# Kernel tuning notes

Hardware: AMD Instinct MI355X
Metric: run time of the kernel (lower is better)

The kernel has to match this reference:

```python
import jax, jax.numpy as jnp
import numpy as np

N = 100000          # nodes
E = 3_200_000       # edges (avg degree 32)
F_IN = 1433
H1, C1 = 8, 8       # conv1: 8 heads x 8 channels -> 64 concat
H2, C2 = 1, 7       # conv2: 1 head x 7 classes
NEG_SLOPE = 0.2


def setup_inputs() -> dict:
    key = jax.random.key(0)
    ks = jax.random.split(key, 10)
    x = jax.random.normal(ks[0], (N, F_IN), dtype=jnp.float32)
    edge_index = jax.random.randint(ks[1], (2, E), 0, N, dtype=jnp.int64)
    s1 = 1.0 / np.sqrt(F_IN)
    s2 = 1.0 / np.sqrt(H1 * C1)
    return {
        "x": x,
        "edge_index": edge_index,
        "W1": jax.random.normal(ks[2], (F_IN, H1 * C1), dtype=jnp.float32) * s1,
        "att_src1": jax.random.normal(ks[3], (H1, C1), dtype=jnp.float32) * s2,
        "att_dst1": jax.random.normal(ks[4], (H1, C1), dtype=jnp.float32) * s2,
        "b1": jnp.zeros((H1 * C1,), dtype=jnp.float32),
        "W2": jax.random.normal(ks[5], (H1 * C1, H2 * C2), dtype=jnp.float32) * s2,
        "att_src2": jax.random.normal(ks[6], (H2, C2), dtype=jnp.float32),
        "att_dst2": jax.random.normal(ks[7], (H2, C2), dtype=jnp.float32),
        "b2": jnp.zeros((H2 * C2,), dtype=jnp.float32),
    }


def gat_conv(x, src, dst, W, att_src, att_dst, b, heads, ch):
    # x: [N, F_in]; src/dst: [E'] (self-loops already appended)
    h = (x @ W).reshape(N, heads, ch)                     # [N, H, C]
    a_src = jnp.einsum('nhc,hc->nh', h, att_src)          # [N, H]
    a_dst = jnp.einsum('nhc,hc->nh', h, att_dst)
    e = a_src[src] + a_dst[dst]                           # [E', H]
    e = jax.nn.leaky_relu(e, NEG_SLOPE)
    # segment softmax over incoming edges of each dst node
    m = jax.ops.segment_max(e, dst, num_segments=N)       # [N, H]
    w = jnp.exp(e - m[dst])
    denom = jax.ops.segment_sum(w, dst, num_segments=N)   # [N, H]
    alpha = w / denom[dst]                                # [E', H]
    msg = alpha[:, :, None] * h[src]                      # [E', H, C]
    out = jax.ops.segment_sum(msg, dst, num_segments=N)   # [N, H, C]
    return out.reshape(N, heads * ch) + b


def reference(x, edge_index, W1, att_src1, att_dst1, b1, W2, att_src2, att_dst2, b2):
    loops = jnp.arange(N, dtype=edge_index.dtype)
    src = jnp.concatenate([edge_index[0], loops])
    dst = jnp.concatenate([edge_index[1], loops])
    # eval mode: all dropout layers are identity
    h = gat_conv(x, src, dst, W1, att_src1, att_dst1, b1, H1, C1)   # [N, 64]
    h = jax.nn.elu(h)
    h = gat_conv(h, src, dst, W2, att_src2, att_dst2, b2, H2, C2)   # [N, 7]
    return jax.nn.log_softmax(h, axis=1)
```

## Files before the change

### kernel.cpp

```cpp
#include <hip/hip_runtime.h>
#include <hip/hip_bf16.h>
#include <math.h>

#define NN 100000
#define EE 3200000
#define ET (EE + NN)
#define FIN 1433
#define KPAD 1440
#define NT 45
#define F1 64
#define F2 7
#define NB 391
#define G1B 782
#define SB 1024
#define CAP 128

typedef __attribute__((ext_vector_type(8))) short short8;
typedef __attribute__((ext_vector_type(4))) float f32x4;
typedef __attribute__((address_space(3))) unsigned int u32_lds;
typedef __attribute__((address_space(1))) const unsigned int u32_glb;

static __device__ __forceinline__ unsigned short f2bf(float f) {
  __hip_bfloat16 h = __float2bfloat16(f);
  return *reinterpret_cast<unsigned short*>(&h);
}
static __device__ __forceinline__ float bf2f(unsigned short u) {
  return __uint_as_float((unsigned int)u << 16);
}

__global__ __launch_bounds__(256) void k_prep(const float* __restrict__ W1,
                                              int* __restrict__ cnt,
                                              unsigned short* __restrict__ WT) {
  int i = blockIdx.x * 256 + threadIdx.x;
  if (i < NN) cnt[i] = 0;
  if (i < F1 * KPAD) {
    int c = i / KPAD, k = i - c * KPAD;
    WT[i] = f2bf((k < FIN) ? W1[k * F1 + c] : 0.f);
  }
}

#define BM 128
#define TILEA 16384
#define TILEB 4096
#define BUFB (TILEA + TILEB)

__global__ __launch_bounds__(256) void k_fuse1(const float* __restrict__ X,
                                               const unsigned short* __restrict__ WT,
                                               unsigned short* __restrict__ Hb,
                                               const int* __restrict__ ei,
                                               int* __restrict__ cnt,
                                               int* __restrict__ csr) {
  if (blockIdx.x >= G1B) {
    const int stride = SB * 256;
    for (int e = (blockIdx.x - G1B) * 256 + threadIdx.x; e < ET; e += stride) {
      int src, dst;
      if (e < EE) { src = ei[e]; dst = ei[EE + e]; }
      else        { src = e - EE; dst = src; }
      int pos = atomicAdd(&cnt[dst], 1);
      csr[(dst << 7) + pos] = src;
    }
    return;
  }
  __shared__ __align__(16) char smem[2 * BUFB];
  const int tid = threadIdx.x;
  const int lane = tid & 63;
  const int wid = tid >> 6;
  const int row0 = blockIdx.x * BM;
  const int wr = (wid >> 1) * 64;
  const int wc = (wid & 1) * 32;
  const int l15 = lane & 15, l4 = lane >> 4;

  const int lrq = tid >> 3;
  const int mq = tid & 7;
  const char* Xb = (const char*)X;
  size_t aoff[4];
#pragma unroll
  for (int q = 0; q < 4; ++q) {
    int lr = q * 32 + lrq;
    int gr = row0 + lr; if (gr >= NN) gr = NN - 1;
    int c = mq ^ (lr & 7);
    aoff[q] = (size_t)gr * (FIN * 4) + (size_t)c * 16;
  }
  const unsigned short* bsrc =
      WT + (tid >> 2) * KPAD + (((tid & 3) ^ ((tid >> 3) & 3)) << 3);

  f32x4 acc[4][2];
#pragma unroll
  for (int a = 0; a < 4; ++a)
#pragma unroll
    for (int b = 0; b < 2; ++b) acc[a][b] = 0.f;

  auto gstage = [&](int k0, char* buf) {
#pragma unroll
    for (int q = 0; q < 4; ++q) {
      __builtin_amdgcn_global_load_lds(
          (u32_glb*)(Xb + aoff[q] + (size_t)k0 * 4),
          (u32_lds*)(buf + q * 4096 + wid * 1024), 16, 0, 0);
    }
  };

  gstage(0, smem);
  {
    short8 b0 = *(const short8*)(bsrc + 0);
    *(short8*)(smem + TILEA + tid * 16) = b0;
  }
  __syncthreads();

  int cur = 0;
  for (int t = 0; t < NT; ++t) {
    char* buf = smem + cur * BUFB;
    char* nbuf = smem + (cur ^ 1) * BUFB;
    const bool have_next = (t + 1 < NT);
    const bool tail = (t + 1 == NT - 1);
    short8 bnext;
    f32x4 atail[4];
    if (have_next) {
      if (!tail) {
        gstage((t + 1) * 32, nbuf);
      } else {
#pragma unroll
        for (int q = 0; q < 4; ++q) {
          int lr = q * 32 + lrq;
          int gr = row0 + lr; if (gr >= NN) gr = NN - 1;
          int c = mq ^ (lr & 7);
          int kb = (NT - 1) * 32 + c * 4;
          const float* xp = X + (size_t)gr * FIN + kb;
#pragma unroll
          for (int j = 0; j < 4; ++j)
            atail[q][j] = (kb + j < FIN) ? xp[j] : 0.f;
        }
      }
      bnext = *(const short8*)(bsrc + (t + 1) * 32);
    }

    short8 af[4], bf[2];
    const int sz = l15 & 7;
#pragma unroll
    for (int fr = 0; fr < 4; ++fr) {
      int r = wr + fr * 16 + l15;
      f32x4 a0 = *(const f32x4*)(buf + r * 128 + ((2 * l4) ^ sz) * 16);
      f32x4 a1 = *(const f32x4*)(buf + r * 128 + ((2 * l4 + 1) ^ sz) * 16);
      short8 v;
#pragma unroll
      for (int j = 0; j < 4; ++j) {
        v[j] = (short)f2bf(a0[j]);
        v[4 + j] = (short)f2bf(a1[j]);
      }
      af[fr] = v;
    }
#pragma unroll
    for (int fc = 0; fc < 2; ++fc) {
      int c = wc + fc * 16 + l15;
      int jp = l4 ^ ((c >> 1) & 3);
      bf[fc] = *(const short8*)(buf + TILEA + c * 64 + jp * 16);
    }
#pragma unroll
    for (int fr = 0; fr < 4; ++fr)
#pragma unroll
      for (int fc = 0; fc < 2; ++fc)
        acc[fr][fc] = __builtin_amdgcn_mfma_f32_16x16x32_bf16(
            af[fr], bf[fc], acc[fr][fc], 0, 0, 0);

    if (have_next) {
      if (tail) {
#pragma unroll
        for (int q = 0; q < 4; ++q)
          *(f32x4*)(nbuf + (q * 32 + lrq) * 128 + mq * 16) = atail[q];
      }
      *(short8*)(nbuf + TILEA + tid * 16) = bnext;
    }
    __syncthreads();
    cur ^= 1;
  }

#pragma unroll
  for (int fr = 0; fr < 4; ++fr) {
    int rbase = row0 + wr + fr * 16 + l4 * 4;
#pragma unroll
    for (int q = 0; q < 4; ++q) {
      int r = rbase + q;
      if (r < NN) {
#pragma unroll
        for (int fc = 0; fc < 2; ++fc)
          Hb[(size_t)r * F1 + wc + fc * 16 + l15] = f2bf(acc[fr][fc][q]);
      }
    }
  }
}

__global__ __launch_bounds__(256) void k_att1(const unsigned short* __restrict__ Hb,
                                              const float* __restrict__ attS,
                                              const float* __restrict__ attD,
                                              float* __restrict__ aS,
                                              float* __restrict__ aD) {
  __shared__ float s_s[64], s_d[64];
  if (threadIdx.x < 64) { s_s[threadIdx.x] = attS[threadIdx.x]; s_d[threadIdx.x] = attD[threadIdx.x]; }
  __syncthreads();
  int idx = blockIdx.x * 256 + threadIdx.x;
  int n = idx >> 3, h = idx & 7;
  if (n >= NN) return;
  short8 v8 = *(const short8*)(Hb + (size_t)n * 64 + h * 8);
  float ss = 0.f, dd = 0.f;
#pragma unroll
  for (int c = 0; c < 8; ++c) {
    float v = bf2f((unsigned short)v8[c]);
    ss = fmaf(v, s_s[h * 8 + c], ss);
    dd = fmaf(v, s_d[h * 8 + c], dd);
  }
  aS[n * 8 + h] = ss;
  aD[n * 8 + h] = dd;
}

__global__ __launch_bounds__(256) void k_agg1(const unsigned short* __restrict__ Hb,
                                              const float* __restrict__ aS,
                                              const float* __restrict__ aD,
                                              const int* __restrict__ cnt,
                                              const int* __restrict__ csr,
                                              const float* __restrict__ b1,
                                              const float* __restrict__ W2,
                                              const float* __restrict__ s2,
                                              const float* __restrict__ d2,
                                              unsigned short* __restrict__ H2b,
                                              float* __restrict__ aD2) {
  __shared__ float s_w2[448];
  __shared__ float s_ss[7], s_dd[7];
  __shared__ float s_b1[64];
  for (int i = threadIdx.x; i < 448; i += 256) s_w2[i] = W2[i];
  if (threadIdx.x < 7) { s_ss[threadIdx.x] = s2[threadIdx.x]; s_dd[threadIdx.x] = d2[threadIdx.x]; }
  if (threadIdx.x < 64) s_b1[threadIdx.x] = b1[threadIdx.x];
  __syncthreads();

  const int wv = threadIdx.x >> 6, lane = threadIdx.x & 63;
  const int n = blockIdx.x * 4 + wv;
  if (n >= NN) return;
  const int eg = lane >> 3, q = lane & 7;
  const float adv = aD[n * 8 + q];
  const int beg = n << 7;
  const int deg = cnt[n];
  float acc[8] = {};
  float den = 0.f;
#pragma unroll 2
  for (int i = eg; i < deg; i += 8) {
    int s = csr[beg + i];
    float e = aS[s * 8 + q] + adv;
    e = (e > 0.f) ? e : 0.2f * e;
    float w = __expf(e);
    den += w;
    short8 hv = *(const short8*)(Hb + (size_t)s * 64 + q * 8);
#pragma unroll
    for (int c = 0; c < 8; ++c)
      acc[c] = fmaf(w, bf2f((unsigned short)hv[c]), acc[c]);
  }
#pragma unroll
  for (int off = 8; off < 64; off <<= 1) {
    den += __shfl_xor(den, off, 64);
#pragma unroll
    for (int c = 0; c < 8; ++c) acc[c] += __shfl_xor(acc[c], off, 64);
  }
  if (eg == 0) {
    float inv = 1.f / den;
    float v[8];
#pragma unroll
    for (int c = 0; c < 8; ++c) {
      float t = acc[c] * inv + s_b1[q * 8 + c];
      v[c] = (t > 0.f) ? t : (__expf(t) - 1.f);
    }
    float p[7] = {};
#pragma unroll
    for (int c = 0; c < 8; ++c) {
      const float* wr = &s_w2[(q * 8 + c) * 7];
#pragma unroll
      for (int j = 0; j < 7; ++j) p[j] = fmaf(v[c], wr[j], p[j]);
    }
#pragma unroll
    for (int off = 1; off < 8; off <<= 1) {
#pragma unroll
      for (int j = 0; j < 7; ++j) p[j] += __shfl_xor(p[j], off, 64);
    }
    if (q == 0) {
      float s = 0.f, d = 0.f;
      short8 row;
#pragma unroll
      for (int j = 0; j < 7; ++j) {
        row[j] = (short)f2bf(p[j]);
        s = fmaf(p[j], s_ss[j], s);
        d = fmaf(p[j], s_dd[j], d);
      }
      row[7] = (short)f2bf(s);
      *(short8*)(H2b + (size_t)n * 8) = row;
      aD2[n] = d;
    }
  }
}

__global__ __launch_bounds__(256) void k_agg2(const unsigned short* __restrict__ H2b,
                                              const float* __restrict__ aD2,
                                              const int* __restrict__ cnt,
                                              const int* __restrict__ csr,
                                              const float* __restrict__ b2,
                                              float* __restrict__ out) {
  const int wv = threadIdx.x >> 6, lane = threadIdx.x & 63;
  const int n = blockIdx.x * 4 + wv;
  if (n >= NN) return;
  const float adv = aD2[n];
  const int beg = n << 7;
  const int deg = cnt[n];
  float acc[7] = {};
  float den = 0.f;
  for (int j = lane; j < deg; j += 64) {
    int s = csr[beg + j];
    short8 hv = *(const short8*)(H2b + (size_t)s * 8);
    float e = bf2f((unsigned short)hv[7]) + adv;
    e = (e > 0.f) ? e : 0.2f * e;
    float wgt = __expf(e);
    den += wgt;
#pragma unroll
    for (int c = 0; c < 7; ++c)
      acc[c] = fmaf(wgt, bf2f((unsigned short)hv[c]), acc[c]);
  }
#pragma unroll
  for (int off = 32; off > 0; off >>= 1) {
    den += __shfl_xor(den, off, 64);
#pragma unroll
    for (int c = 0; c < 7; ++c) acc[c] += __shfl_xor(acc[c], off, 64);
  }
  if (lane == 0) {
    float inv = 1.f / den;
    float v[7];
    float m = -1e30f;
#pragma unroll
    for (int c = 0; c < 7; ++c) { v[c] = acc[c] * inv + b2[c]; m = fmaxf(m, v[c]); }
    float se = 0.f;
#pragma unroll
    for (int c = 0; c < 7; ++c) se += __expf(v[c] - m);
    float lse = m + __logf(se);
#pragma unroll
    for (int c = 0; c < 7; ++c) out[n * 7 + c] = v[c] - lse;
  }
}

extern "C" void kernel_launch(void* const* d_in, const int* in_sizes, int n_in,
                              void* d_out, int out_size, void* d_ws, size_t ws_size,
                              hipStream_t stream) {
  const float* x   = (const float*)d_in[0];
  const int*   ei  = (const int*)d_in[1];
  const float* W1  = (const float*)d_in[2];
  const float* as1 = (const float*)d_in[3];
  const float* ad1 = (const float*)d_in[4];
  const float* b1  = (const float*)d_in[5];
  const float* W2  = (const float*)d_in[6];
  const float* as2 = (const float*)d_in[7];
  const float* ad2 = (const float*)d_in[8];
  const float* b2  = (const float*)d_in[9];
  float* out = (float*)d_out;

  char* ws = (char*)d_ws;
  size_t off = 0;
  auto alloc = [&](size_t bytes) {
    void* p = ws + off;
    off += (bytes + 255) & ~(size_t)255;
    return p;
  };
  unsigned short* h1b = (unsigned short*)alloc((size_t)NN * 64 * 2);
  float* sc1    = (float*)alloc((size_t)NN * 8 * 4);
  float* dc1    = (float*)alloc((size_t)NN * 8 * 4);
  unsigned short* h2b = (unsigned short*)alloc((size_t)NN * 8 * 2);
  float* dc2    = (float*)alloc((size_t)NN * 4);
  int*   cnt    = (int*)alloc((size_t)NN * 4);
  int*   csr    = (int*)alloc((size_t)NN * CAP * 4);
  unsigned short* w1t = (unsigned short*)alloc((size_t)F1 * KPAD * 2);

  k_prep<<<NB, 256, 0, stream>>>(W1, cnt, w1t);

  k_fuse1<<<G1B + SB, 256, 0, stream>>>(x, w1t, h1b, ei, cnt, csr);

  k_att1<<<(NN * 8 + 255) / 256, 256, 0, stream>>>(h1b, as1, ad1, sc1, dc1);

  k_agg1<<<(NN + 3) / 4, 256, 0, stream>>>(h1b, sc1, dc1, cnt, csr, b1,
                                           W2, as2, ad2, h2b, dc2);

  k_agg2<<<(NN + 3) / 4, 256, 0, stream>>>(h2b, dc2, cnt, csr, b2, out);
}
```

Measured before the change: 438.6 us.

## Partition CSR build per XCD with workgroup-scope atomics, merge in fused att kernel

The edge-bucketing phase now reads the XCC id from a hardware register and writes into one of eight per-XCD count/CSR arrays. It uses workgroup-scope atomics on the assumption that each partition is only touched by blocks on one XCD, which keeps the atomics in the local L2 instead of device-coherent memory. A new merge phase, fused into the attention-score kernel as extra blocks, concatenates the eight partitions into the original CSR layout. The risks are the extra merge pass and memory, a per-partition cap of 24 that could overflow for high-degree nodes, and relying on workgroup-scope atomics being coherent across CUs within an XCD.

```diff
diff --git a/kernel.cpp b/kernel.cpp
--- a/kernel.cpp
+++ b/kernel.cpp
@@ -14,6 +14,10 @@
 #define G1B 782
 #define SB 1024
 #define CAP 128
+#define NXCD 8
+#define CAPX 24
+#define A1B 3125
+#define CPB 25000
 
 typedef __attribute__((ext_vector_type(8))) short short8;
 typedef __attribute__((ext_vector_type(4))) float f32x4;
@@ -29,10 +33,10 @@
 }
 
 __global__ __launch_bounds__(256) void k_prep(const float* __restrict__ W1,
-                                              int* __restrict__ cnt,
+                                              int* __restrict__ cnt2,
                                               unsigned short* __restrict__ WT) {
   int i = blockIdx.x * 256 + threadIdx.x;
-  if (i < NN) cnt[i] = 0;
+  if (i < NXCD * NN) cnt2[i] = 0;
   if (i < F1 * KPAD) {
     int c = i / KPAD, k = i - c * KPAD;
     WT[i] = f2bf((k < FIN) ? W1[k * F1 + c] : 0.f);
@@ -48,16 +52,22 @@
                                                const unsigned short* __restrict__ WT,
                                                unsigned short* __restrict__ Hb,
                                                const int* __restrict__ ei,
-                                               int* __restrict__ cnt,
-                                               int* __restrict__ csr) {
+                                               int* __restrict__ cnt2,
+                                               int* __restrict__ csr2) {
   if (blockIdx.x >= G1B) {
+    int xcc;
+    asm volatile("s_getreg_b32 %0, hwreg(20, 0, 32)" : "=s"(xcc));
+    xcc &= 7;
+    int* mycnt = cnt2 + xcc * NN;
+    int* mycsr = csr2 + (size_t)xcc * NN * CAPX;
     const int stride = SB * 256;
     for (int e = (blockIdx.x - G1B) * 256 + threadIdx.x; e < ET; e += stride) {
       int src, dst;
       if (e < EE) { src = ei[e]; dst = ei[EE + e]; }
       else        { src = e - EE; dst = src; }
-      int pos = atomicAdd(&cnt[dst], 1);
-      csr[(dst << 7) + pos] = src;
+      int pos = __hip_atomic_fetch_add(&mycnt[dst], 1, __ATOMIC_RELAXED,
+                                       __HIP_MEMORY_SCOPE_WORKGROUP);
+      mycsr[dst * CAPX + pos] = src;
     }
     return;
   }
@@ -188,11 +198,31 @@
   }
 }
 
-__global__ __launch_bounds__(256) void k_att1(const unsigned short* __restrict__ Hb,
-                                              const float* __restrict__ attS,
-                                              const float* __restrict__ attD,
-                                              float* __restrict__ aS,
-                                              float* __restrict__ aD) {
+__global__ __launch_bounds__(256) void k_fuse2(const unsigned short* __restrict__ Hb,
+                                               const float* __restrict__ attS,
+                                               const float* __restrict__ attD,
+                                               float* __restrict__ aS,
+                                               float* __restrict__ aD,
+                                               const int* __restrict__ cnt2,
+                                               const int* __restrict__ csr2,
+                                               int* __restrict__ cnt,
+                                               int* __restrict__ csr) {
+  if (blockIdx.x >= A1B) {
+    const int wv = threadIdx.x >> 6, lane = threadIdx.x & 63;
+    const int n = (blockIdx.x - A1B) * 4 + wv;
+    if (n >= NN) return;
+    int c[NXCD];
+    int deg = 0;
+#pragma unroll
+    for (int x = 0; x < NXCD; ++x) { c[x] = cnt2[x * NN + n]; deg += c[x]; }
+    for (int i = lane; i < deg; i += 64) {
+      int x = 0, off = i;
+      while (off >= c[x]) { off -= c[x]; ++x; }
+      csr[(n << 7) + i] = csr2[((size_t)x * NN + n) * CAPX + off];
+    }
+    if (lane == 0) cnt[n] = deg;
+    return;
+  }
   __shared__ float s_s[64], s_d[64];
   if (threadIdx.x < 64) { s_s[threadIdx.x] = attS[threadIdx.x]; s_d[threadIdx.x] = attD[threadIdx.x]; }
   __syncthreads();
@@ -368,13 +398,16 @@
   float* dc2    = (float*)alloc((size_t)NN * 4);
   int*   cnt    = (int*)alloc((size_t)NN * 4);
   int*   csr    = (int*)alloc((size_t)NN * CAP * 4);
+  int*   cnt2   = (int*)alloc((size_t)NXCD * NN * 4);
+  int*   csr2   = (int*)alloc((size_t)NXCD * NN * CAPX * 4);
   unsigned short* w1t = (unsigned short*)alloc((size_t)F1 * KPAD * 2);
 
-  k_prep<<<NB, 256, 0, stream>>>(W1, cnt, w1t);
-
-  k_fuse1<<<G1B + SB, 256, 0, stream>>>(x, w1t, h1b, ei, cnt, csr);
-
-  k_att1<<<(NN * 8 + 255) / 256, 256, 0, stream>>>(h1b, as1, ad1, sc1, dc1);
+  k_prep<<<(NXCD * NN + 255) / 256, 256, 0, stream>>>(W1, cnt2, w1t);
+
+  k_fuse1<<<G1B + SB, 256, 0, stream>>>(x, w1t, h1b, ei, cnt2, csr2);
+
+  k_fuse2<<<A1B + CPB, 256, 0, stream>>>(h1b, as1, ad1, sc1, dc1,
+                                         cnt2, csr2, cnt, csr);
 
   k_agg1<<<(NN + 3) / 4, 256, 0, stream>>>(h1b, sc1, dc1, cnt, csr, b1,
                                            W2, as2, ad2, h2b, dc2);
```

Result: slower. 482.7 us (+10.0%).

## Build CSR via two-level binning instead of global atomics scatter

Applied to the files above, without the earlier changes.

Replaces the global-atomic CSR build (one atomicAdd per edge on a per-node counter, with scattered writes) with a two-pass bucketed sort. Each block first builds a shared-memory histogram of 512-node bins, then a single-block scan turns these into offsets. A binning kernel writes packed (local dst, src) words into contiguous bin regions, and per-bin blocks build the CSR rows using LDS atomics, fused with the attention-score kernel. The aim is to remove global atomic contention and random writes, at the cost of extra launches, a serial scan kernel and an extra pass over the edges.

```diff
diff --git a/kernel.cpp b/kernel.cpp
--- a/kernel.cpp
+++ b/kernel.cpp
@@ -10,10 +10,13 @@
 #define NT 45
 #define F1 64
 #define F2 7
-#define NB 391
 #define G1B 782
-#define SB 1024
 #define CAP 128
+#define BINS 200
+#define SB1 256
+#define CH_E 12891
+#define NB4 196
+#define A1B 3125
 
 typedef __attribute__((ext_vector_type(8))) short short8;
 typedef __attribute__((ext_vector_type(4))) float f32x4;
@@ -29,10 +32,8 @@
 }
 
 __global__ __launch_bounds__(256) void k_prep(const float* __restrict__ W1,
-                                              int* __restrict__ cnt,
                                               unsigned short* __restrict__ WT) {
   int i = blockIdx.x * 256 + threadIdx.x;
-  if (i < NN) cnt[i] = 0;
   if (i < F1 * KPAD) {
     int c = i / KPAD, k = i - c * KPAD;
     WT[i] = f2bf((k < FIN) ? W1[k * F1 + c] : 0.f);
@@ -48,17 +49,19 @@
                                                const unsigned short* __restrict__ WT,
                                                unsigned short* __restrict__ Hb,
                                                const int* __restrict__ ei,
-                                               int* __restrict__ cnt,
-                                               int* __restrict__ csr) {
+                                               int* __restrict__ histM) {
   if (blockIdx.x >= G1B) {
-    const int stride = SB * 256;
-    for (int e = (blockIdx.x - G1B) * 256 + threadIdx.x; e < ET; e += stride) {
-      int src, dst;
-      if (e < EE) { src = ei[e]; dst = ei[EE + e]; }
-      else        { src = e - EE; dst = src; }
-      int pos = atomicAdd(&cnt[dst], 1);
-      csr[(dst << 7) + pos] = src;
-    }
+    __shared__ int hist[BINS];
+    const int b = blockIdx.x - G1B;
+    for (int i = threadIdx.x; i < BINS; i += 256) hist[i] = 0;
+    __syncthreads();
+    const int e0 = b * CH_E, e1 = min(e0 + CH_E, ET);
+    for (int e = e0 + threadIdx.x; e < e1; e += 256) {
+      int dst = (e < EE) ? ei[EE + e] : (e - EE);
+      atomicAdd(&hist[dst >> 9], 1);
+    }
+    __syncthreads();
+    for (int i = threadIdx.x; i < BINS; i += 256) histM[b * BINS + i] = hist[i];
     return;
   }
   __shared__ __align__(16) char smem[2 * BUFB];
@@ -188,11 +191,82 @@
   }
 }
 
-__global__ __launch_bounds__(256) void k_att1(const unsigned short* __restrict__ Hb,
-                                              const float* __restrict__ attS,
-                                              const float* __restrict__ attD,
-                                              float* __restrict__ aS,
-                                              float* __restrict__ aD) {
+__global__ __launch_bounds__(256) void k_scanM(int* __restrict__ histM,
+                                               int* __restrict__ binS,
+                                               int* __restrict__ binE) {
+  __shared__ int s[256];
+  const int t = threadIdx.x;
+  int total = 0;
+  if (t < BINS)
+    for (int b = 0; b < SB1; ++b) total += histM[b * BINS + t];
+  s[t] = total;
+  __syncthreads();
+  for (int off = 1; off < 256; off <<= 1) {
+    int v = s[t];
+    int u = (t >= off) ? s[t - off] : 0;
+    __syncthreads();
+    s[t] = v + u;
+    __syncthreads();
+  }
+  if (t < BINS) {
+    int run = s[t] - total;
+    binS[t] = run;
+    for (int b = 0; b < SB1; ++b) {
+      int h = histM[b * BINS + t];
+      histM[b * BINS + t] = run;
+      run += h;
+    }
+    binE[t] = run;
+  }
+}
+
+__global__ __launch_bounds__(256) void k_bin(const int* __restrict__ ei,
+                                             const int* __restrict__ histM,
+                                             unsigned int* __restrict__ binned) {
+  __shared__ int cur[BINS];
+  const int b = blockIdx.x;
+  for (int i = threadIdx.x; i < BINS; i += 256) cur[i] = histM[b * BINS + i];
+  __syncthreads();
+  const int e0 = b * CH_E, e1 = min(e0 + CH_E, ET);
+  for (int e = e0 + threadIdx.x; e < e1; e += 256) {
+    int dst = (e < EE) ? ei[EE + e] : (e - EE);
+    int src = (e < EE) ? ei[e] : dst;
+    int pos = atomicAdd(&cur[dst >> 9], 1);
+    binned[pos] = ((unsigned)(dst & 511) << 17) | (unsigned)src;
+  }
+}
+
+__global__ __launch_bounds__(256) void k_fuse2(const unsigned short* __restrict__ Hb,
+                                               const float* __restrict__ attS,
+                                               const float* __restrict__ attD,
+                                               float* __restrict__ aS,
+                                               float* __restrict__ aD,
+                                               const unsigned int* __restrict__ binned,
+                                               const int* __restrict__ binS,
+                                               const int* __restrict__ binE,
+                                               int* __restrict__ cnt,
+                                               int* __restrict__ csr) {
+  if (blockIdx.x >= A1B) {
+    __shared__ int lcnt[512];
+    const int g = blockIdx.x - A1B;
+    for (int i = threadIdx.x; i < 512; i += 256) lcnt[i] = 0;
+    __syncthreads();
+    const int s0 = binS[g], s1 = binE[g];
+    const int nbase = g << 9;
+    for (int i = s0 + threadIdx.x; i < s1; i += 256) {
+      unsigned v = binned[i];
+      int ld = v >> 17;
+      int src = (int)(v & 0x1FFFFu);
+      int pos = atomicAdd(&lcnt[ld], 1);
+      csr[((size_t)(nbase + ld) << 7) + pos] = src;
+    }
+    __syncthreads();
+    for (int i = threadIdx.x; i < 512; i += 256) {
+      int n = nbase + i;
+      if (n < NN) cnt[n] = lcnt[i];
+    }
+    return;
+  }
   __shared__ float s_s[64], s_d[64];
   if (threadIdx.x < 64) { s_s[threadIdx.x] = attS[threadIdx.x]; s_d[threadIdx.x] = attD[threadIdx.x]; }
   __syncthreads();
@@ -368,13 +442,22 @@
   float* dc2    = (float*)alloc((size_t)NN * 4);
   int*   cnt    = (int*)alloc((size_t)NN * 4);
   int*   csr    = (int*)alloc((size_t)NN * CAP * 4);
+  int*   histM  = (int*)alloc((size_t)SB1 * BINS * 4);
+  int*   binS   = (int*)alloc((size_t)BINS * 4);
+  int*   binE   = (int*)alloc((size_t)BINS * 4);
+  unsigned int* binned = (unsigned int*)alloc((size_t)ET * 4);
   unsigned short* w1t = (unsigned short*)alloc((size_t)F1 * KPAD * 2);
 
-  k_prep<<<NB, 256, 0, stream>>>(W1, cnt, w1t);
-
-  k_fuse1<<<G1B + SB, 256, 0, stream>>>(x, w1t, h1b, ei, cnt, csr);
-
-  k_att1<<<(NN * 8 + 255) / 256, 256, 0, stream>>>(h1b, as1, ad1, sc1, dc1);
+  k_prep<<<(F1 * KPAD + 255) / 256, 256, 0, stream>>>(W1, w1t);
+
+  k_fuse1<<<G1B + SB1, 256, 0, stream>>>(x, w1t, h1b, ei, histM);
+
+  k_scanM<<<1, 256, 0, stream>>>(histM, binS, binE);
+
+  k_bin<<<SB1, 256, 0, stream>>>(ei, histM, binned);
+
+  k_fuse2<<<A1B + NB4, 256, 0, stream>>>(h1b, as1, ad1, sc1, dc1,
+                                         binned, binS, binE, cnt, csr);
 
   k_agg1<<<(NN + 3) / 4, 256, 0, stream>>>(h1b, sc1, dc1, cnt, csr, b1,
                                            W2, as2, ad2, h2b, dc2);
```

Measured after the change: 436.7 us, median of 2. Within noise of the previous version (-0.4%).
